# Kernel optimization log

Hardware: AMD Instinct MI355X
Metric: run time of the kernel (lower is better)

The kernel has to match this reference:

```python
import jax, jax.numpy as jnp
import numpy as np

B, H, W, C = 16, 64, 64, 256
WIN, SHIFT, HEADS, NSTYLE, HID = 8, 4, 8, 512, 1024
HB = HEADS // 2   # heads per attention branch
CB = C // 2       # channels per branch
N = WIN * WIN     # tokens per window
EPS = 1e-5


def _rel_index(w):
    coords = np.stack(np.meshgrid(np.arange(w), np.arange(w), indexing='ij'))  # [2,w,w]
    cf = coords.reshape(2, -1)
    rel = (cf[:, :, None] - cf[:, None, :]).transpose(1, 2, 0)  # [N,N,2]
    rel[:, :, 0] += w - 1
    rel[:, :, 1] += w - 1
    rel[:, :, 0] *= 2 * w - 1
    return rel.sum(-1)  # [N,N]


def _sw_mask(Hh, Ww, w, shift):
    img = np.zeros((Hh, Ww))
    cnt = 0
    for hs in (slice(0, -w), slice(-w, -shift), slice(-shift, None)):
        for ws in (slice(0, -w), slice(-w, -shift), slice(-shift, None)):
            img[hs, ws] = cnt
            cnt += 1
    win = img.reshape(Hh // w, w, Ww // w, w).transpose(0, 2, 1, 3).reshape(-1, w * w)
    m = win[:, None, :] - win[:, :, None]
    return np.where(m != 0, -100.0, 0.0).astype(np.float32)  # [nW,N,N]


REL_IDX = _rel_index(WIN)
SW_MASK = jnp.asarray(_sw_mask(H, W, WIN, SHIFT))


def window_partition(x):
    # x: [B,H,W,c] -> [B*nW, N, c]
    b, hh, ww, c = x.shape
    x = x.reshape(b, hh // WIN, WIN, ww // WIN, WIN, c).transpose(0, 1, 3, 2, 4, 5)
    return x.reshape(-1, N, c)


def window_reverse(win):
    c = win.shape[-1]
    x = win.reshape(B, H // WIN, W // WIN, WIN, WIN, c).transpose(0, 1, 3, 2, 4, 5)
    return x.reshape(B, H, W, c)


def _adain(x, style, Wa, ba):
    # x: [B,L,C]; instance norm over L per channel, then style affine
    s = style @ Wa + ba                      # [B, 2C]
    mu_s, std_s = jnp.split(s, 2, axis=1)    # each [B,C]
    mu = x.mean(axis=1, keepdims=True)
    var = ((x - mu) ** 2).mean(axis=1, keepdims=True)
    xn = (x - mu) * jax.lax.rsqrt(var + EPS)
    return mu_s[:, None, :] + std_s[:, None, :] * xn


def _win_attn(q, k, v, rpb, mask):
    # q,k,v: [B_, N, CB]; rpb: [(2w-1)^2, HB]; mask: [nW,N,N] or None
    B_ = q.shape[0]
    d = CB // HB
    q = q.reshape(B_, N, HB, d).transpose(0, 2, 1, 3) * (d ** -0.5)
    k = k.reshape(B_, N, HB, d).transpose(0, 2, 1, 3)
    v = v.reshape(B_, N, HB, d).transpose(0, 2, 1, 3)
    attn = jnp.einsum('bhnd,bhmd->bhnm', q, k)
    bias = rpb[REL_IDX.reshape(-1)].reshape(N, N, HB).transpose(2, 0, 1)
    attn = attn + bias[None]
    if mask is not None:
        nW = mask.shape[0]
        attn = attn.reshape(B_ // nW, nW, HB, N, N) + mask[None, :, None]
        attn = attn.reshape(B_, HB, N, N)
    attn = jax.nn.softmax(attn, axis=-1)
    out = jnp.einsum('bhnm,bhmd->bhnd', attn, v)
    return out.transpose(0, 2, 1, 3).reshape(B_, N, CB)


def setup_inputs() -> dict:
    key = jax.random.key(0)
    ks = jax.random.split(key, 20)
    f = jnp.float32
    return {
        'x': jax.random.normal(ks[0], (B, H * W, C), f),
        'style': jax.random.normal(ks[1], (B, NSTYLE), f),
        'w_qkv': jax.random.normal(ks[2], (C, 3 * C), f) * 0.02,
        'b_qkv': jnp.zeros((3 * C,), f),
        'w_proj': jax.random.normal(ks[3], (C, C), f) * 0.02,
        'b_proj': jnp.zeros((C,), f),
        'w_ada1': jax.random.normal(ks[4], (NSTYLE, 2 * C), f) * 0.02,
        'b_ada1': jnp.concatenate([jnp.zeros((C,), f), jnp.ones((C,), f)]),
        'w_ada2': jax.random.normal(ks[5], (NSTYLE, 2 * C), f) * 0.02,
        'b_ada2': jnp.concatenate([jnp.zeros((C,), f), jnp.ones((C,), f)]),
        'rpb1': jax.random.normal(ks[6], ((2 * WIN - 1) ** 2, HB), f) * 0.02,
        'rpb2': jax.random.normal(ks[7], ((2 * WIN - 1) ** 2, HB), f) * 0.02,
        'w_fc1': jax.random.normal(ks[8], (C, HID), f) * 0.02,
        'b_fc1': jnp.zeros((HID,), f),
        'w_fc2': jax.random.normal(ks[9], (HID, C), f) * 0.02,
        'b_fc2': jnp.zeros((C,), f),
    }


def reference(x, style, w_qkv, b_qkv, w_proj, b_proj, w_ada1, b_ada1,
              w_ada2, b_ada2, rpb1, rpb2, w_fc1, b_fc1, w_fc2, b_fc2):
    Bn, L, Cc = x.shape
    # AdaIN 1
    h = _adain(x, style, w_ada1, b_ada1)                      # [B,L,C]
    qkv = (h @ w_qkv + b_qkv).reshape(Bn, H, W, 3, Cc)
    q, k, v = qkv[..., 0, :], qkv[..., 1, :], qkv[..., 2, :]  # [B,H,W,C]
    # split channels across the two branches
    q1, k1, v1 = q[..., :CB], k[..., :CB], v[..., :CB]
    q2, k2, v2 = q[..., CB:], k[..., CB:], v[..., CB:]
    shift = lambda t: jnp.roll(t, (-SHIFT, -SHIFT), axis=(1, 2))
    # W-MSA branch
    x_w = _win_attn(window_partition(q1), window_partition(k1),
                    window_partition(v1), rpb1, None)
    # SW-MSA branch (shifted windows + mask)
    x_sw = _win_attn(window_partition(shift(q2)), window_partition(shift(k2)),
                     window_partition(shift(v2)), rpb2, SW_MASK)
    xw = window_reverse(x_w)                                  # [B,H,W,CB]
    xsw = jnp.roll(window_reverse(x_sw), (SHIFT, SHIFT), axis=(1, 2))
    attn_out = jnp.concatenate([xw, xsw], axis=-1).reshape(Bn, L, Cc)
    x = x + attn_out @ w_proj + b_proj
    # AdaIN 2 + MLP (exact GELU, as nn.GELU default)
    h2 = _adain(x, style, w_ada2, b_ada2)
    h2 = jax.nn.gelu(h2 @ w_fc1 + b_fc1, approximate=False)
    return x + (h2 @ w_fc2 + b_fc2)
```

## Files before the change

### kernel.cpp

```cpp
#include <hip/hip_runtime.h>
#include <hip/hip_bf16.h>

typedef __bf16 bf16;
typedef __bf16 bf16x4v __attribute__((ext_vector_type(4)));
typedef __bf16 bf16x8v __attribute__((ext_vector_type(8)));
typedef float f32x4 __attribute__((ext_vector_type(4)));
typedef short s16x4 __attribute__((ext_vector_type(4)));

#define DEVINL static __device__ __forceinline__

DEVINL f32x4 mfma16(bf16x8v a, bf16x8v b, f32x4 c) {
  return __builtin_amdgcn_mfma_f32_16x16x32_bf16(a, b, c, 0, 0, 0);
}

DEVINL f32x4 mfma16x16(bf16x4v a, bf16x4v b, f32x4 c) {
#if __has_builtin(__builtin_amdgcn_mfma_f32_16x16x16bf16_1k)
  return __builtin_amdgcn_mfma_f32_16x16x16bf16_1k(
      __builtin_bit_cast(s16x4, a), __builtin_bit_cast(s16x4, b), c, 0, 0, 0);
#else
  f32x4 d;
  asm("v_mfma_f32_16x16x16_bf16 %0, %1, %2, %3"
      : "=v"(d) : "v"(a), "v"(b), "v"(c));
  return d;
#endif
}

__global__ __launch_bounds__(256) void k_style(
    const float* __restrict__ style,
    const float* __restrict__ wa1, const float* __restrict__ ba1,
    const float* __restrict__ wa2, const float* __restrict__ ba2,
    float* __restrict__ s1, float* __restrict__ s2) {
  int idx = blockIdx.x * 256 + threadIdx.x;
  int which = idx >> 13;
  int r = idx & 8191;
  int b = r >> 9, n = r & 511;
  const float* wa = which ? wa2 : wa1;
  const float* ba = which ? ba2 : ba1;
  const float* srow = style + b * 512;
  float acc = ba[n];
  for (int k = 0; k < 512; ++k)
    acc += srow[k] * wa[k * 512 + n];
  (which ? s2 : s1)[b * 512 + n] = acc;
}

template<int F32>
__global__ __launch_bounds__(256) void k_stats_part(
    const void* __restrict__ xv, float* __restrict__ psum,
    float* __restrict__ psq) {
  int rc = blockIdx.x, b = blockIdx.y;
  int c = threadIdx.x;
  size_t base = (size_t)b * 4096 * 256 + (size_t)rc * 256 * 256 + c;
  float sm = 0.f, q = 0.f;
  #pragma unroll 4
  for (int r = 0; r < 256; ++r) {
    float f;
    if constexpr (F32) f = ((const float*)xv)[base + (size_t)r * 256];
    else               f = (float)((const bf16*)xv)[base + (size_t)r * 256];
    sm += f; q += f * f;
  }
  int o = (b * 16 + rc) * 256 + c;
  psum[o] = sm; psq[o] = q;
}

__global__ __launch_bounds__(256) void k_stats_fin(
    const float* __restrict__ psum, const float* __restrict__ psq,
    const float* __restrict__ s,
    float* __restrict__ scale, float* __restrict__ shift) {
  int b = blockIdx.x, c = threadIdx.x;
  float S = 0.f, Q = 0.f;
  #pragma unroll
  for (int rc = 0; rc < 16; ++rc) {
    S += psum[(b * 16 + rc) * 256 + c];
    Q += psq[(b * 16 + rc) * 256 + c];
  }
  float mean = S * (1.0f/4096.0f);
  float var  = Q * (1.0f/4096.0f) - mean * mean;
  float inv  = rsqrtf(var + 1e-5f);
  float mu_s  = s[b * 512 + c];
  float std_s = s[b * 512 + 256 + c];
  float sc = std_s * inv;
  scale[b * 256 + c] = sc;
  shift[b * 256 + c] = mu_s - sc * mean;
}

template<int F32>
__global__ __launch_bounds__(256) void k_adain(
    const void* __restrict__ in, const float* __restrict__ scale,
    const float* __restrict__ shift, bf16* __restrict__ out) {
  int idx = blockIdx.x * 256 + threadIdx.x;
  int c8 = idx & 31, row = idx >> 5;
  int b = row >> 12, c = c8 * 8;
  const float* scp = &scale[b * 256 + c];
  const float* shp = &shift[b * 256 + c];
  f32x4 sc0 = *(const f32x4*)scp, sc1 = *(const f32x4*)(scp + 4);
  f32x4 sh0 = *(const f32x4*)shp, sh1 = *(const f32x4*)(shp + 4);
  size_t ofs = (size_t)row * 256 + c;
  float f[8];
  if constexpr (F32) {
    f32x4 v0 = *(const f32x4*)&((const float*)in)[ofs];
    f32x4 v1 = *(const f32x4*)&((const float*)in)[ofs + 4];
    f[0]=v0[0]; f[1]=v0[1]; f[2]=v0[2]; f[3]=v0[3];
    f[4]=v1[0]; f[5]=v1[1]; f[6]=v1[2]; f[7]=v1[3];
  } else {
    bf16x8v v = *(const bf16x8v*)&((const bf16*)in)[ofs];
    #pragma unroll
    for (int u = 0; u < 8; ++u) f[u] = (float)v[u];
  }
  bf16x8v o;
  o[0]=(bf16)(sh0[0]+sc0[0]*f[0]); o[1]=(bf16)(sh0[1]+sc0[1]*f[1]);
  o[2]=(bf16)(sh0[2]+sc0[2]*f[2]); o[3]=(bf16)(sh0[3]+sc0[3]*f[3]);
  o[4]=(bf16)(sh1[0]+sc1[0]*f[4]); o[5]=(bf16)(sh1[1]+sc1[1]*f[5]);
  o[6]=(bf16)(sh1[2]+sc1[2]*f[6]); o[7]=(bf16)(sh1[3]+sc1[3]*f[7]);
  *(bf16x8v*)&out[ofs] = o;
}

__global__ __launch_bounds__(256) void k_tr(
    const float* __restrict__ in, bf16* __restrict__ out, int K, int N) {
  __shared__ float t[32][33];
  int bx = blockIdx.x * 32, by = blockIdx.y * 32;
  int tx = threadIdx.x & 31, ty = threadIdx.x >> 5;
  #pragma unroll
  for (int r = 0; r < 32; r += 8)
    t[ty + r][tx] = in[(size_t)(by + ty + r) * N + bx + tx];
  __syncthreads();
  #pragma unroll
  for (int r = 0; r < 32; r += 8)
    out[(size_t)(bx + ty + r) * K + by + tx] = (bf16)t[tx][ty + r];
}

DEVINL void stage_lds(bf16* dst, const bf16* __restrict__ src, int ld,
                      int row0, int k0, int tid) {
  int w = tid >> 6, l = tid & 63;
  #pragma unroll
  for (int i = 0; i < 4; ++i) {
    int slot = i * 256 + w * 64 + l;
    int r = slot >> 3, cs = slot & 7;
    int c = cs ^ (r & 7);
    const bf16* g = src + (size_t)(row0 + r) * ld + k0 + c * 8;
    __builtin_amdgcn_global_load_lds(
        (const __attribute__((address_space(1))) void*)g,
        (__attribute__((address_space(3))) void*)(dst + (i * 256 + w * 64) * 8),
        16, 0, 0);
  }
}

template<int RESMODE, int GELU, int OUTF32>
__global__ __launch_bounds__(256) void k_gemm(
    const bf16* __restrict__ A, const bf16* __restrict__ Bt,
    const float* __restrict__ bias, const void* __restrict__ resv,
    void* __restrict__ outv, int N, int K, int gx) {
  __shared__ bf16 a_sw[128 * 64];
  __shared__ bf16 b_sw[128 * 64];
  int tid = threadIdx.x;
  int l = tid & 63, w = tid >> 6;
  int wr = w >> 1, wc = w & 1;
  int lm = l & 15, lg = l >> 4;

  int nwg = gridDim.x;
  int lin = blockIdx.x;
  int swz = (lin & 7) * (nwg >> 3) + (lin >> 3);
  int bx = swz % gx, by = swz / gx;
  int m0 = by * 128, n0 = bx * 128;

  f32x4 acc[4][4];
  #pragma unroll
  for (int mi = 0; mi < 4; ++mi)
    #pragma unroll
    for (int ni = 0; ni < 4; ++ni)
      acc[mi][ni] = (f32x4){0.f, 0.f, 0.f, 0.f};

  for (int k0 = 0; k0 < K; k0 += 64) {
    stage_lds(a_sw, A, K, m0, k0, tid);
    stage_lds(b_sw, Bt, K, n0, k0, tid);
    __syncthreads();
    #pragma unroll
    for (int kk = 0; kk < 2; ++kk) {
      bf16x8v af[4], bv[4];
      #pragma unroll
      for (int mi = 0; mi < 4; ++mi) {
        int row = wr * 64 + mi * 16 + lm;
        af[mi] = *(const bf16x8v*)&a_sw[row * 64 + (((kk * 4 + lg) ^ (row & 7)) * 8)];
      }
      #pragma unroll
      for (int ni = 0; ni < 4; ++ni) {
        int row = wc * 64 + ni * 16 + lm;
        bv[ni] = *(const bf16x8v*)&b_sw[row * 64 + (((kk * 4 + lg) ^ (row & 7)) * 8)];
      }
      #pragma unroll
      for (int mi = 0; mi < 4; ++mi)
        #pragma unroll
        for (int ni = 0; ni < 4; ++ni)
          acc[mi][ni] = mfma16(af[mi], bv[ni], acc[mi][ni]);
    }
    __syncthreads();
  }
  #pragma unroll
  for (int mi = 0; mi < 4; ++mi) {
    #pragma unroll
    for (int ni = 0; ni < 4; ++ni) {
      int row = m0 + wr * 64 + mi * 16 + lg * 4;
      int col = n0 + wc * 64 + ni * 16 + lm;
      float bv_ = bias[col];
      #pragma unroll
      for (int j = 0; j < 4; ++j) {
        float o = acc[mi][ni][j] + bv_;
        if constexpr (RESMODE == 1)
          o += ((const float*)resv)[(size_t)(row + j) * N + col];
        if constexpr (RESMODE == 2)
          o += (float)((const bf16*)resv)[(size_t)(row + j) * N + col];
        if constexpr (GELU)
          o = 0.5f * o * (1.0f + erff(o * 0.70710678118654752f));
        if constexpr (OUTF32)
          ((float*)outv)[(size_t)(row + j) * N + col] = o;
        else
          ((bf16*)outv)[(size_t)(row + j) * N + col] = (bf16)o;
      }
    }
  }
}

__global__ __launch_bounds__(256) void k_attn(
    const bf16* __restrict__ qkv,
    const float* __restrict__ rpb1, const float* __restrict__ rpb2,
    bf16* __restrict__ aout) {
  __shared__ bf16 vt[128 * 72];
  __shared__ float rl[960];

  int tid = threadIdx.x;
  int bx = blockIdx.x;
  int br = bx & 1, widx = (bx >> 1) & 63, b = bx >> 7;
  int wy = widx >> 3, wx = widx & 7;

  const float* rpb = br ? rpb2 : rpb1;
  #pragma unroll
  for (int t = tid; t < 960; t += 256) {
    int h0 = t / 240, r0 = t - h0 * 240, dy = r0 >> 4, dx = r0 & 15;
    rl[t] = (dx < 15) ? rpb[(dy * 15 + dx) * 4 + h0] : 0.f;
  }

  auto grow = [&](int tok) -> int {
    int y = wy * 8 + (tok >> 3), xc = wx * 8 + (tok & 7);
    if (br) { y = (y + 4) & 63; xc = (xc + 4) & 63; }
    return b * 4096 + y * 64 + xc;
  };

  #pragma unroll
  for (int it = 0; it < 4; ++it) {
    int task = it * 256 + tid;
    int tok = task & 63, chunk = task >> 6;
    bf16x8v v = *(const bf16x8v*)&qkv[(size_t)grow(tok) * 768 + 512 + br * 128 + chunk * 8];
    #pragma unroll
    for (int u = 0; u < 8; ++u) vt[(chunk * 8 + u) * 72 + tok] = v[u];
  }

  int l = tid & 63, h = tid >> 6;
  int lm = l & 15, lg = l >> 4;

  bf16x8v kb[4], qa[4];
  #pragma unroll
  for (int i = 0; i < 4; ++i) {
    size_t rb = (size_t)grow(i * 16 + lm) * 768 + br * 128 + h * 32 + lg * 8;
    qa[i] = *(const bf16x8v*)&qkv[rb];
    kb[i] = *(const bf16x8v*)&qkv[rb + 256];
  }
  __syncthreads();

  bf16x4v vb[2][4];
  #pragma unroll
  for (int ni = 0; ni < 2; ++ni)
    #pragma unroll
    for (int ki = 0; ki < 4; ++ki)
      vb[ni][ki] = *(const bf16x4v*)&vt[(h * 32 + ni * 16 + lm) * 72 + ki * 16 + lg * 4];

  bool need_mask = br && (wy == 7 || wx == 7);

  int ekA[16], idkA[16];
  #pragma unroll
  for (int ki = 0; ki < 4; ++ki)
    #pragma unroll
    for (int j = 0; j < 4; ++j) {
      int ik = ki * 16 + lg * 4 + j;
      ekA[ki * 4 + j] = ik + (ik >> 3) * 8;
      int yk = wy * 8 + (ik >> 3), xk = wx * 8 + (ik & 7);
      idkA[ki * 4 + j] = (yk < 56 ? 0 : (yk < 60 ? 1 : 2)) * 3
                       + (xk < 56 ? 0 : (xk < 60 ? 1 : 2));
    }

  #pragma unroll
  for (int qi = 0; qi < 4; ++qi) {
    f32x4 s[4];
    #pragma unroll
    for (int ki = 0; ki < 4; ++ki)
      s[ki] = mfma16(kb[ki], qa[qi], (f32x4){0.f,0.f,0.f,0.f});

    int iq = qi * 16 + lm;
    int eq = iq + (iq >> 3) * 8;
    int yq = wy * 8 + (iq >> 3), xq = wx * 8 + (iq & 7);
    int idq = (yq < 56 ? 0 : (yq < 60 ? 1 : 2)) * 3
            + (xq < 56 ? 0 : (xq < 60 ? 1 : 2));
    const float* fb = &rl[h * 240 + 119 + eq];

    #pragma unroll
    for (int ki = 0; ki < 4; ++ki)
      #pragma unroll
      for (int j = 0; j < 4; ++j) {
        float val = s[ki][j] * 0.17677669529663687f + fb[-ekA[ki * 4 + j]];
        if (need_mask && idq != idkA[ki * 4 + j]) val -= 100.0f;
        s[ki][j] = val;
      }

    float mx = s[0][0];
    #pragma unroll
    for (int ki = 0; ki < 4; ++ki)
      #pragma unroll
      for (int j = 0; j < 4; ++j) mx = fmaxf(mx, s[ki][j]);
    mx = fmaxf(mx, __shfl_xor(mx, 16));
    mx = fmaxf(mx, __shfl_xor(mx, 32));
    float sum = 0.f;
    #pragma unroll
    for (int ki = 0; ki < 4; ++ki)
      #pragma unroll
      for (int j = 0; j < 4; ++j) {
        float e = __expf(s[ki][j] - mx);
        s[ki][j] = e;
        sum += e;
      }
    sum += __shfl_xor(sum, 16);
    sum += __shfl_xor(sum, 32);
    float rs = 1.0f / sum;

    bf16x4v pa[4];
    #pragma unroll
    for (int ki = 0; ki < 4; ++ki)
      #pragma unroll
      for (int j = 0; j < 4; ++j)
        pa[ki][j] = (bf16)(s[ki][j] * rs);

    f32x4 o[2] = {(f32x4){0.f,0.f,0.f,0.f}, (f32x4){0.f,0.f,0.f,0.f}};
    #pragma unroll
    for (int ki = 0; ki < 4; ++ki) {
      o[0] = mfma16x16(pa[ki], vb[0][ki], o[0]);
      o[1] = mfma16x16(pa[ki], vb[1][ki], o[1]);
    }

    #pragma unroll
    for (int ni = 0; ni < 2; ++ni)
      #pragma unroll
      for (int j = 0; j < 4; ++j) {
        int tok = qi * 16 + lg * 4 + j;
        int col = br * 128 + h * 32 + ni * 16 + lm;
        aout[(size_t)grow(tok) * 256 + col] = (bf16)o[ni][j];
      }
  }
}

extern "C" void kernel_launch(void* const* d_in, const int* in_sizes, int n_in,
                              void* d_out, int out_size, void* d_ws, size_t ws_size,
                              hipStream_t stream) {
  (void)in_sizes; (void)n_in; (void)out_size; (void)ws_size;
  const float* x      = (const float*)d_in[0];
  const float* style  = (const float*)d_in[1];
  const float* w_qkv  = (const float*)d_in[2];
  const float* b_qkv  = (const float*)d_in[3];
  const float* w_proj = (const float*)d_in[4];
  const float* b_proj = (const float*)d_in[5];
  const float* w_ada1 = (const float*)d_in[6];
  const float* b_ada1 = (const float*)d_in[7];
  const float* w_ada2 = (const float*)d_in[8];
  const float* b_ada2 = (const float*)d_in[9];
  const float* rpb1   = (const float*)d_in[10];
  const float* rpb2   = (const float*)d_in[11];
  const float* w_fc1  = (const float*)d_in[12];
  const float* b_fc1  = (const float*)d_in[13];
  const float* w_fc2  = (const float*)d_in[14];
  const float* b_fc2  = (const float*)d_in[15];

  char* ws = (char*)d_ws;
  float* s1     = (float*)(ws + 0);
  float* s2     = (float*)(ws + 32768);
  float* scale1 = (float*)(ws + 65536);
  float* shift1 = (float*)(ws + 81920);
  float* scale2 = (float*)(ws + 98304);
  float* shift2 = (float*)(ws + 114688);
  bf16* wtqkv   = (bf16*)(ws + 131072);
  bf16* wtproj  = (bf16*)(ws + 524288);
  bf16* wtfc1   = (bf16*)(ws + 655360);
  bf16* wtfc2   = (bf16*)(ws + 1179648);
  float* psum   = (float*)(ws + 1703936);
  float* psq    = (float*)(ws + 1966080);
  const size_t BIG = 2228224;
  bf16* xn   = (bf16*)(ws + BIG);
  bf16* qkv  = (bf16*)(ws + BIG + 33554432);
  bf16* attn = (bf16*)(ws + BIG + 134217728);
  bf16* x1   = (bf16*)(ws + BIG + 33554432);
  bf16* xn2  = xn;
  bf16* g    = (bf16*)(ws + BIG + 67108864);

  k_tr<<<dim3(24, 8),  256, 0, stream>>>(w_qkv,  wtqkv,  256, 768);
  k_tr<<<dim3(8, 8),   256, 0, stream>>>(w_proj, wtproj, 256, 256);
  k_tr<<<dim3(32, 8),  256, 0, stream>>>(w_fc1,  wtfc1,  256, 1024);
  k_tr<<<dim3(8, 32),  256, 0, stream>>>(w_fc2,  wtfc2,  1024, 256);

  k_style<<<64, 256, 0, stream>>>(style, w_ada1, b_ada1, w_ada2, b_ada2, s1, s2);
  k_stats_part<1><<<dim3(16, 16), 256, 0, stream>>>(x, psum, psq);
  k_stats_fin<<<16, 256, 0, stream>>>(psum, psq, s1, scale1, shift1);
  k_adain<1><<<8192, 256, 0, stream>>>(x, scale1, shift1, xn);

  k_gemm<0,0,0><<<3072, 256, 0, stream>>>(
      xn, wtqkv, b_qkv, nullptr, qkv, 768, 256, 6);

  k_attn<<<2048, 256, 0, stream>>>(qkv, rpb1, rpb2, attn);

  k_gemm<1,0,0><<<1024, 256, 0, stream>>>(
      attn, wtproj, b_proj, x, x1, 256, 256, 2);

  k_stats_part<0><<<dim3(16, 16), 256, 0, stream>>>(x1, psum, psq);
  k_stats_fin<<<16, 256, 0, stream>>>(psum, psq, s2, scale2, shift2);
  k_adain<0><<<8192, 256, 0, stream>>>(x1, scale2, shift2, xn2);

  for (int ch = 0; ch < 2; ++ch) {
    size_t ro = (size_t)ch * 32768;
    k_gemm<0,1,0><<<2048, 256, 0, stream>>>(
        xn2 + ro * 256, wtfc1, b_fc1, nullptr, g, 1024, 256, 8);
    k_gemm<2,0,1><<<512, 256, 0, stream>>>(
        g, wtfc2, b_fc2, x1 + ro * 256,
        (float*)d_out + ro * 256, 256, 1024, 2);
  }
}
```

Before: 341.9 us.

## Double-buffer GEMM LDS tiles to overlap global loads with MFMA compute

The GEMM kernel now keeps two LDS buffer pairs and prefetches the next K-tile with global_load_lds while MFMAs run on the current tile. This cuts the per-iteration barrier count from two to one and is meant to hide global-memory latency behind compute. Tile source addresses are computed once, outside the loop. LDS use per block doubles to 64KB, which may reduce how many blocks fit on each CU.

```diff
diff --git a/kernel.cpp b/kernel.cpp
--- a/kernel.cpp
+++ b/kernel.cpp
@@ -128,29 +128,12 @@
     out[(size_t)(bx + ty + r) * K + by + tx] = (bf16)t[tx][ty + r];
 }
 
-DEVINL void stage_lds(bf16* dst, const bf16* __restrict__ src, int ld,
-                      int row0, int k0, int tid) {
-  int w = tid >> 6, l = tid & 63;
-  #pragma unroll
-  for (int i = 0; i < 4; ++i) {
-    int slot = i * 256 + w * 64 + l;
-    int r = slot >> 3, cs = slot & 7;
-    int c = cs ^ (r & 7);
-    const bf16* g = src + (size_t)(row0 + r) * ld + k0 + c * 8;
-    __builtin_amdgcn_global_load_lds(
-        (const __attribute__((address_space(1))) void*)g,
-        (__attribute__((address_space(3))) void*)(dst + (i * 256 + w * 64) * 8),
-        16, 0, 0);
-  }
-}
-
 template<int RESMODE, int GELU, int OUTF32>
 __global__ __launch_bounds__(256) void k_gemm(
     const bf16* __restrict__ A, const bf16* __restrict__ Bt,
     const float* __restrict__ bias, const void* __restrict__ resv,
     void* __restrict__ outv, int N, int K, int gx) {
-  __shared__ bf16 a_sw[128 * 64];
-  __shared__ bf16 b_sw[128 * 64];
+  __shared__ bf16 sm[4][128 * 64];
   int tid = threadIdx.x;
   int l = tid & 63, w = tid >> 6;
   int wr = w >> 1, wc = w & 1;
@@ -162,6 +145,19 @@
   int bx = swz % gx, by = swz / gx;
   int m0 = by * 128, n0 = bx * 128;
 
+  const bf16* asrc[4];
+  const bf16* bsrc[4];
+  int ldso[4];
+  #pragma unroll
+  for (int i = 0; i < 4; ++i) {
+    int slot = i * 256 + w * 64 + l;
+    int r = slot >> 3, cs = slot & 7;
+    int c = cs ^ (r & 7);
+    asrc[i] = A  + (size_t)(m0 + r) * K + c * 8;
+    bsrc[i] = Bt + (size_t)(n0 + r) * K + c * 8;
+    ldso[i] = (i * 256 + w * 64) * 8;
+  }
+
   f32x4 acc[4][4];
   #pragma unroll
   for (int mi = 0; mi < 4; ++mi)
@@ -169,22 +165,48 @@
     for (int ni = 0; ni < 4; ++ni)
       acc[mi][ni] = (f32x4){0.f, 0.f, 0.f, 0.f};
 
-  for (int k0 = 0; k0 < K; k0 += 64) {
-    stage_lds(a_sw, A, K, m0, k0, tid);
-    stage_lds(b_sw, Bt, K, n0, k0, tid);
-    __syncthreads();
+  int nt = K >> 6;
+  int cur = 0;
+
+  #pragma unroll
+  for (int i = 0; i < 4; ++i) {
+    __builtin_amdgcn_global_load_lds(
+        (const __attribute__((address_space(1))) void*)asrc[i],
+        (__attribute__((address_space(3))) void*)&sm[0][ldso[i]], 16, 0, 0);
+    __builtin_amdgcn_global_load_lds(
+        (const __attribute__((address_space(1))) void*)bsrc[i],
+        (__attribute__((address_space(3))) void*)&sm[1][ldso[i]], 16, 0, 0);
+  }
+  __syncthreads();
+
+  for (int t = 0; t < nt; ++t) {
+    if (t + 1 < nt) {
+      int k1 = (t + 1) << 6;
+      int nb = (cur ^ 1) << 1;
+      #pragma unroll
+      for (int i = 0; i < 4; ++i) {
+        __builtin_amdgcn_global_load_lds(
+            (const __attribute__((address_space(1))) void*)(asrc[i] + k1),
+            (__attribute__((address_space(3))) void*)&sm[nb][ldso[i]], 16, 0, 0);
+        __builtin_amdgcn_global_load_lds(
+            (const __attribute__((address_space(1))) void*)(bsrc[i] + k1),
+            (__attribute__((address_space(3))) void*)&sm[nb + 1][ldso[i]], 16, 0, 0);
+      }
+    }
+    const bf16* as_ = sm[cur << 1];
+    const bf16* bs_ = sm[(cur << 1) + 1];
     #pragma unroll
     for (int kk = 0; kk < 2; ++kk) {
       bf16x8v af[4], bv[4];
       #pragma unroll
       for (int mi = 0; mi < 4; ++mi) {
         int row = wr * 64 + mi * 16 + lm;
-        af[mi] = *(const bf16x8v*)&a_sw[row * 64 + (((kk * 4 + lg) ^ (row & 7)) * 8)];
+        af[mi] = *(const bf16x8v*)&as_[row * 64 + (((kk * 4 + lg) ^ (row & 7)) * 8)];
       }
       #pragma unroll
       for (int ni = 0; ni < 4; ++ni) {
         int row = wc * 64 + ni * 16 + lm;
-        bv[ni] = *(const bf16x8v*)&b_sw[row * 64 + (((kk * 4 + lg) ^ (row & 7)) * 8)];
+        bv[ni] = *(const bf16x8v*)&bs_[row * 64 + (((kk * 4 + lg) ^ (row & 7)) * 8)];
       }
       #pragma unroll
       for (int mi = 0; mi < 4; ++mi)
@@ -192,8 +214,12 @@
         for (int ni = 0; ni < 4; ++ni)
           acc[mi][ni] = mfma16(af[mi], bv[ni], acc[mi][ni]);
     }
-    __syncthreads();
-  }
+    if (t + 1 < nt) {
+      __syncthreads();
+      cur ^= 1;
+    }
+  }
+
   #pragma unroll
   for (int mi = 0; mi < 4; ++mi) {
     #pragma unroll
```

Measured after the change: 354.6 us. 3.7% more time.
